# Optimization experiments

Measured on AMD Instinct MI355X. Metric: run time of the kernel, lower is better.

## Reference

```python
import jax, jax.numpy as jnp
import numpy as np

B, T, H = 16, 2048, 1024   # batch, time, hidden_dim
G, V, D = 2, 320, 128      # num_codebooks, codebook_size, codebook_dim
TAU = 1.0                  # gumbel-softmax temperature (forward default)
EPS = 1e-9


def setup_inputs() -> dict:
    key = jax.random.key(0)
    ks = jax.random.split(key, 6)
    return {
        "x": jax.random.normal(ks[0], (B, T, H), jnp.float32),
        "W_in": jax.random.normal(ks[1], (G * V, H), jnp.float32) / np.sqrt(H),
        "b_in": jnp.zeros((G * V,), jnp.float32),
        "codebook": jax.random.uniform(ks[2], (G, V, D), jnp.float32),
        "W_out": jax.random.normal(ks[3], (H, G * D), jnp.float32) / np.sqrt(G * D),
        "b_out": jnp.zeros((H,), jnp.float32),
        "gumbel_u": jax.random.uniform(ks[4], (B, T, G, V), jnp.float32,
                                       minval=1e-6, maxval=1.0 - 1e-6),
    }


def reference(x, W_in, b_in, codebook, W_out, b_out, gumbel_u):
    # input projection -> per-group logits [B,T,G,V]
    logits = (x @ W_in.T + b_in).reshape(B, T, G, V)
    # gumbel-softmax (soft, training path)
    gumbels = -jnp.log(-jnp.log(gumbel_u))
    probs = jax.nn.softmax((logits + gumbels) / TAU, axis=-1)
    # perplexity over average code usage
    avg_probs = probs.mean(axis=(0, 1))  # [G,V]
    perplexity = jnp.exp(-(avg_probs * jnp.log(avg_probs + EPS)).sum(-1)).mean()
    # quantize: soft mixture over codebook, concat groups, project out
    q = jnp.einsum('btgv,gvd->btgd', probs, codebook).reshape(B, T, G * D)
    q = q @ W_out.T + b_out  # [B,T,H]
    commit_loss = jnp.mean((x - jax.lax.stop_gradient(q)) ** 2)
    return (q, perplexity, commit_loss)
```

## Files before the change

### kernel.cpp

```cpp
#include <hip/hip_runtime.h>

typedef unsigned short ushort_t;
typedef unsigned int uint_t;
typedef __attribute__((ext_vector_type(4))) float f32x4;
typedef __attribute__((ext_vector_type(8))) short bf16x8;

#define B_   16
#define T_   2048
#define H_   1024
#define G_   2
#define V_   320
#define D_   128
#define NT   32768
#define GV   640
#define GD   256

#define LGKM0() asm volatile("s_waitcnt lgkmcnt(0)" ::: "memory")
#define BAR()   __builtin_amdgcn_s_barrier()
#define GLDS16(g, l) __builtin_amdgcn_global_load_lds( \
    (const __attribute__((address_space(1))) void*)(g), \
    (__attribute__((address_space(3))) void*)(l), 16, 0, 0)

__device__ __forceinline__ ushort_t cvt_bf16(float f) {
  uint_t u = __float_as_uint(f);
  uint_t r = (u + 0x7FFFu + ((u >> 16) & 1u)) >> 16;
  return (ushort_t)r;
}

__device__ __forceinline__ bf16x8 pack8(f32x4 a, f32x4 b) {
  union { uint_t u[4]; bf16x8 v; } r;
  asm("v_cvt_pk_bf16_f32 %0, %1, %2" : "=v"(r.u[0]) : "v"(a[0]), "v"(a[1]));
  asm("v_cvt_pk_bf16_f32 %0, %1, %2" : "=v"(r.u[1]) : "v"(a[2]), "v"(a[3]));
  asm("v_cvt_pk_bf16_f32 %0, %1, %2" : "=v"(r.u[2]) : "v"(b[0]), "v"(b[1]));
  asm("v_cvt_pk_bf16_f32 %0, %1, %2" : "=v"(r.u[3]) : "v"(b[2]), "v"(b[3]));
  return r.v;
}

__global__ void pq_prep(const float* __restrict__ W_in, const float* __restrict__ W_out,
                        const float* __restrict__ cb, ushort_t* __restrict__ winb,
                        ushort_t* __restrict__ woutb, ushort_t* __restrict__ cbp,
                        float* __restrict__ avg_g, float* __restrict__ closs,
                        uint_t* __restrict__ counter) {
  int idx = blockIdx.x * 256 + threadIdx.x;
  const int N1 = GV * H_;
  const int N2 = H_ * GD;
  const int N3 = 81920;
  if (idx < N1) { winb[idx] = cvt_bf16(W_in[idx]); return; }
  idx -= N1;
  if (idx < N2) { woutb[idx] = cvt_bf16(W_out[idx]); return; }
  idx -= N2;
  if (idx < N3) {
    int g = idx / 40960;
    int r = idx % 40960;
    int kk = r / 4096;
    int r2 = r % 4096;
    int n  = r2 >> 9;
    int ln = (r2 >> 3) & 63;
    int i  = r2 & 7;
    int v = kk * 32 + (ln >> 4) * 8 + i;
    int d = n * 16 + (ln & 15);
    cbp[idx] = cvt_bf16(cb[((size_t)g * V_ + v) * D_ + d]);
    return;
  }
  idx -= N3;
  if (idx < GV) { avg_g[idx] = 0.f; return; }
  idx -= GV;
  if (idx == 0) { *closs = 0.f; *counter = 0u; }
}

__global__ __launch_bounds__(256, 2) void pq_kA(
    const float* __restrict__ x, const float* __restrict__ b_in,
    const float* __restrict__ gum, const ushort_t* __restrict__ winb,
    const ushort_t* __restrict__ cbp, ushort_t* __restrict__ qmid,
    float* __restrict__ avg_g) {
  __shared__ char smem[43520];
  char* sBbuf = smem;
  char* sP    = smem;
  float* sAvg = (float*)(smem + 40960);

  const int tid = threadIdx.x;
  const int lane = tid & 63;
  const int wid = tid >> 6;
  const int wm = wid;
  const int g  = blockIdx.x & 1;
  const int lo = lane & 15;
  const int hi = lane >> 4;
  const int row0 = (blockIdx.x >> 1) * 128;

  for (int i = tid; i < V_; i += 256) sAvg[i] = 0.f;

  const int bV   = wid * 80 + (lane >> 2);
  const int bCc  = (lane & 3) ^ ((lane >> 3) & 3);
  const ushort_t* bSrc0 = winb + (size_t)(g * 320 + bV) * H_ + bCc * 8;

  const float* xr0 = x + (size_t)(row0 + wm * 32 + lo) * H_ + hi * 8;
  const float* xr1 = xr0 + (size_t)16 * H_;

  f32x4 acc[2][20];
#pragma unroll
  for (int m = 0; m < 2; ++m)
#pragma unroll
    for (int n = 0; n < 20; ++n) acc[m][n] = (f32x4){0.f, 0.f, 0.f, 0.f};

  __syncthreads();

#define STAGEB(buf, kb)                                                         \
  do {                                                                          \
    char* lb = sBbuf + (buf) * 20480 + wid * 5120;                              \
    const ushort_t* bs = bSrc0 + (kb);                                          \
    GLDS16(bs,             lb);                                                 \
    GLDS16(bs + 16 * H_,   lb + 1024);                                          \
    GLDS16(bs + 32 * H_,   lb + 2048);                                          \
    GLDS16(bs + 48 * H_,   lb + 3072);                                          \
    GLDS16(bs + 64 * H_,   lb + 4096);                                          \
  } while (0)

  STAGEB(0, 0);
  f32x4 xa0 = *reinterpret_cast<const f32x4*>(xr0);
  f32x4 xa1 = *reinterpret_cast<const f32x4*>(xr0 + 4);
  f32x4 xb0 = *reinterpret_cast<const f32x4*>(xr1);
  f32x4 xb1 = *reinterpret_cast<const f32x4*>(xr1 + 4);

  const int swzB = (lo >> 1) & 3;

#pragma unroll 1
  for (int ks = 0; ks < 32; ++ks) {
    if (ks < 31) {
      STAGEB((ks + 1) & 1, (ks + 1) * 32);
      asm volatile("s_waitcnt vmcnt(5)" ::: "memory");
    } else {
      asm volatile("s_waitcnt vmcnt(0)" ::: "memory");
    }
    BAR();

    bf16x8 af0 = pack8(xa0, xa1);
    bf16x8 af1 = pack8(xb0, xb1);

    if (ks < 31) {
      const int ko = (ks + 1) * 32;
      xa0 = *reinterpret_cast<const f32x4*>(xr0 + ko);
      xa1 = *reinterpret_cast<const f32x4*>(xr0 + ko + 4);
      xb0 = *reinterpret_cast<const f32x4*>(xr1 + ko);
      xb1 = *reinterpret_cast<const f32x4*>(xr1 + ko + 4);
    }

    const char* cB = sBbuf + (ks & 1) * 20480;
#pragma unroll
    for (int n = 0; n < 20; ++n) {
      const int v = n * 16 + lo;
      bf16x8 bf = *reinterpret_cast<const bf16x8*>(cB + v * 64 + ((hi ^ swzB) * 16));
      acc[0][n] = __builtin_amdgcn_mfma_f32_16x16x32_bf16(af0, bf, acc[0][n], 0, 0, 0);
      acc[1][n] = __builtin_amdgcn_mfma_f32_16x16x32_bf16(af1, bf, acc[1][n], 0, 0, 0);
    }
    LGKM0();
    BAR();
  }
#undef STAGEB

  float bias[20];
#pragma unroll
  for (int n = 0; n < 20; ++n) bias[n] = b_in[g * 320 + n * 16 + lo];

#pragma unroll
  for (int mrep = 0; mrep < 2; ++mrep) {
#pragma unroll
    for (int j = 0; j < 4; ++j) {
      const int trow = row0 + wm * 32 + mrep * 16 + hi * 4 + j;
      const float* up = gum + ((size_t)trow * G_ + g) * V_;
      float zmax = -3.0e38f;
#pragma unroll
      for (int n = 0; n < 20; ++n) {
        float u = up[n * 16 + lo];
        float gv = -__logf(-__logf(u));
        float z = acc[mrep][n][j] + bias[n] + gv;
        acc[mrep][n][j] = z;
        zmax = fmaxf(zmax, z);
      }
#pragma unroll
      for (int mk = 1; mk <= 8; mk <<= 1) zmax = fmaxf(zmax, __shfl_xor(zmax, mk));
      float s = 0.f;
#pragma unroll
      for (int n = 0; n < 20; ++n) {
        float p = __expf(acc[mrep][n][j] - zmax);
        acc[mrep][n][j] = p;
        s += p;
      }
#pragma unroll
      for (int mk = 1; mk <= 8; mk <<= 1) s += __shfl_xor(s, mk);
      float inv = 1.f / s;
#pragma unroll
      for (int n = 0; n < 20; ++n) acc[mrep][n][j] *= inv;
    }
#pragma unroll
    for (int n = 0; n < 20; ++n) {
      float cs = acc[mrep][n][0] + acc[mrep][n][1] + acc[mrep][n][2] + acc[mrep][n][3];
      cs += __shfl_xor(cs, 16);
      cs += __shfl_xor(cs, 32);
      if (hi == 0) atomicAdd(&sAvg[n * 16 + lo], cs);
    }
#pragma unroll
    for (int n = 0; n < 20; ++n) {
#pragma unroll
      for (int j = 0; j < 4; ++j) {
        float v = acc[mrep][n][j];
        float pv = __shfl_xor(v, 1);
        if ((lane & 1) == 0) {
          uint_t w = (uint_t)cvt_bf16(v) | ((uint_t)cvt_bf16(pv) << 16);
          int prow = wm * 16 + hi * 4 + j;
          int byte = prow * 640 + (((n * 16 + lo) * 2) ^ ((prow & 7) << 4));
          *reinterpret_cast<uint_t*>(sP + byte) = w;
        }
      }
    }
    LGKM0();
    f32x4 acc2[8];
#pragma unroll
    for (int n = 0; n < 8; ++n) acc2[n] = (f32x4){0.f, 0.f, 0.f, 0.f};
#pragma unroll
    for (int kk = 0; kk < 10; ++kk) {
      int prow = wm * 16 + lo;
      int byte = prow * 640 + ((kk * 64 + hi * 16) ^ ((prow & 7) << 4));
      bf16x8 ap = *reinterpret_cast<const bf16x8*>(sP + byte);
#pragma unroll
      for (int n = 0; n < 8; ++n) {
        bf16x8 bc = *reinterpret_cast<const bf16x8*>(cbp + ((size_t)((g * 10 + kk) * 8 + n) * 64 + lane) * 8);
        acc2[n] = __builtin_amdgcn_mfma_f32_16x16x32_bf16(ap, bc, acc2[n], 0, 0, 0);
      }
    }
#pragma unroll
    for (int n = 0; n < 8; ++n) {
#pragma unroll
      for (int j = 0; j < 4; ++j) {
        float v = acc2[n][j];
        float pv = __shfl_xor(v, 1);
        if ((lane & 1) == 0) {
          uint_t w = (uint_t)cvt_bf16(v) | ((uint_t)cvt_bf16(pv) << 16);
          int trow = row0 + wm * 32 + mrep * 16 + hi * 4 + j;
          *reinterpret_cast<uint_t*>(qmid + (size_t)trow * GD + g * 128 + n * 16 + lo) = w;
        }
      }
    }
  }
  __syncthreads();
  for (int i = tid; i < V_; i += 256) atomicAdd(&avg_g[g * 320 + i], sAvg[i]);
}

__global__ __launch_bounds__(512, 2) void pq_kB(
    const ushort_t* __restrict__ qmid, const ushort_t* __restrict__ woutb,
    const float* __restrict__ b_out, const float* __restrict__ x,
    float* __restrict__ out, float* __restrict__ closs,
    const float* __restrict__ avg_g, uint_t* __restrict__ counter) {
  __shared__ char smem[49152 + 64];
  __shared__ int sLast;
  char* sA = smem;
  char* sB = smem + 16384;
  float* sRed = (float*)(smem + 49152);

  const int tid = threadIdx.x;
  const int lane = tid & 63;
  const int wid = tid >> 6;
  const int wm = wid >> 2;
  const int wn = wid & 3;
  const int lo = lane & 15, hi = lane >> 4;
  const int tm = blockIdx.x >> 2;
  const int tn = blockIdx.x & 3;
  const int row0 = tm * 128;
  const int col0 = tn * 256;

  f32x4 acc[4][4];
#pragma unroll
  for (int mr = 0; mr < 4; ++mr)
#pragma unroll
    for (int nr = 0; nr < 4; ++nr) acc[mr][nr] = (f32x4){0.f, 0.f, 0.f, 0.f};

  for (int ks = 0; ks < 4; ++ks) {
    const int kb = ks * 64;
#pragma unroll
    for (int u = 0; u < 2; ++u) {
      int s = u * 512 + tid;
      int r = s >> 3, c = s & 7;
      uint4 wv = *reinterpret_cast<const uint4*>(qmid + (size_t)(row0 + r) * GD + kb + c * 8);
      int byte = (r * 128 + c * 16) ^ ((r & 7) << 4);
      *reinterpret_cast<uint4*>(sA + byte) = wv;
    }
#pragma unroll
    for (int u = 0; u < 4; ++u) {
      int s = u * 512 + tid;
      int r = s >> 3, c = s & 7;
      uint4 wv = *reinterpret_cast<const uint4*>(woutb + (size_t)(col0 + r) * GD + kb + c * 8);
      int byte = (r * 128 + c * 16) ^ ((r & 7) << 4);
      *reinterpret_cast<uint4*>(sB + byte) = wv;
    }
    __syncthreads();
#pragma unroll
    for (int kk = 0; kk < 2; ++kk) {
      bf16x8 af[4], bf[4];
#pragma unroll
      for (int mr = 0; mr < 4; ++mr) {
        int row = wm * 64 + mr * 16 + lo;
        int byte = (row * 128 + kk * 64 + hi * 16) ^ ((row & 7) << 4);
        af[mr] = *reinterpret_cast<const bf16x8*>(sA + byte);
      }
#pragma unroll
      for (int nr = 0; nr < 4; ++nr) {
        int col = wn * 64 + nr * 16 + lo;
        int byte = (col * 128 + kk * 64 + hi * 16) ^ ((col & 7) << 4);
        bf[nr] = *reinterpret_cast<const bf16x8*>(sB + byte);
      }
#pragma unroll
      for (int mr = 0; mr < 4; ++mr)
#pragma unroll
        for (int nr = 0; nr < 4; ++nr)
          acc[mr][nr] = __builtin_amdgcn_mfma_f32_16x16x32_bf16(af[mr], bf[nr], acc[mr][nr], 0, 0, 0);
    }
    __syncthreads();
  }
  float bias[4];
#pragma unroll
  for (int nr = 0; nr < 4; ++nr) bias[nr] = b_out[col0 + wn * 64 + nr * 16 + lo];
  float csum = 0.f;
#pragma unroll
  for (int mr = 0; mr < 4; ++mr)
#pragma unroll
    for (int nr = 0; nr < 4; ++nr)
#pragma unroll
      for (int j = 0; j < 4; ++j) {
        int row = row0 + wm * 64 + mr * 16 + hi * 4 + j;
        int col = col0 + wn * 64 + nr * 16 + lo;
        float q = acc[mr][nr][j] + bias[nr];
        out[(size_t)row * H_ + col] = q;
        float d = x[(size_t)row * H_ + col] - q;
        csum += d * d;
      }
#pragma unroll
  for (int mk = 1; mk <= 32; mk <<= 1) csum += __shfl_xor(csum, mk);
  if (lane == 0) sRed[wid] = csum;
  __syncthreads();
  if (tid == 0) {
    float t = 0.f;
    for (int w = 0; w < 8; ++w) t += sRed[w];
    atomicAdd(closs, t);
    __threadfence();
    uint_t c = atomicAdd(counter, 1u);
    sLast = (c == 1023u) ? 1 : 0;
  }
  __syncthreads();
  if (sLast && tid < 64) {
    float a0 = 0.f, a1 = 0.f;
    for (int v = tid; v < V_; v += 64) {
      float p0 = avg_g[v] * (1.f / (float)NT);
      a0 += p0 * __logf(p0 + 1e-9f);
      float p1 = avg_g[V_ + v] * (1.f / (float)NT);
      a1 += p1 * __logf(p1 + 1e-9f);
    }
#pragma unroll
    for (int mk = 1; mk <= 32; mk <<= 1) { a0 += __shfl_xor(a0, mk); a1 += __shfl_xor(a1, mk); }
    if (tid == 0) {
      float cl = atomicAdd(closs, 0.0f);
      out[(size_t)NT * H_]     = 0.5f * (__expf(-a0) + __expf(-a1));
      out[(size_t)NT * H_ + 1] = cl * (1.f / ((float)NT * (float)H_));
    }
  }
}

extern "C" void kernel_launch(void* const* d_in, const int* in_sizes, int n_in,
                              void* d_out, int out_size, void* d_ws, size_t ws_size,
                              hipStream_t stream) {
  const float* x     = (const float*)d_in[0];
  const float* W_in  = (const float*)d_in[1];
  const float* b_in  = (const float*)d_in[2];
  const float* cb    = (const float*)d_in[3];
  const float* W_out = (const float*)d_in[4];
  const float* b_out = (const float*)d_in[5];
  const float* gum   = (const float*)d_in[6];
  float* out = (float*)d_out;

  char* ws = (char*)d_ws;
  ushort_t* winb  = (ushort_t*)ws;
  ushort_t* woutb = (ushort_t*)(ws + 1310720);
  ushort_t* cbp   = (ushort_t*)(ws + 1835008);
  float*    avg_g = (float*)(ws + 1998848);
  float*    closs = (float*)(ws + 2001408);
  uint_t*   cnt   = (uint_t*)(ws + 2001472);
  ushort_t* qmid  = (ushort_t*)(ws + 2001920);

  pq_prep<<<3907, 256, 0, stream>>>(W_in, W_out, cb, winb, woutb, cbp, avg_g, closs, cnt);
  pq_kA<<<512, 256, 0, stream>>>(x, b_in, gum, winb, cbp, qmid, avg_g);
  pq_kB<<<1024, 512, 0, stream>>>(qmid, woutb, b_out, x, out, closs, avg_g, cnt);
}
```

Before: 245.1 us.

## Transpose logits MFMA so each lane owns one row for softmax

Swaps the MFMA operand order in the logits GEMM, so each lane now holds four consecutive vocab entries of a single token row instead of four rows. Softmax max and sum then need only two cross-lane shuffles per row, and the gumbel noise and bias are read as float4 vectors instead of scalar loads. Probabilities are packed straight to bf16 with v_cvt_pk into the swizzled LDS tile, with no shuffle-and-pair step. The column sums for avg_probs now take a 4-step shuffle reduction per element, which may add shuffle work in exchange.

```diff
diff --git a/kernel.cpp b/kernel.cpp
--- a/kernel.cpp
+++ b/kernel.cpp
@@ -27,12 +27,18 @@
   return (ushort_t)r;
 }
 
+__device__ __forceinline__ uint_t cvtpk(float a, float b) {
+  uint_t r;
+  asm("v_cvt_pk_bf16_f32 %0, %1, %2" : "=v"(r) : "v"(a), "v"(b));
+  return r;
+}
+
 __device__ __forceinline__ bf16x8 pack8(f32x4 a, f32x4 b) {
   union { uint_t u[4]; bf16x8 v; } r;
-  asm("v_cvt_pk_bf16_f32 %0, %1, %2" : "=v"(r.u[0]) : "v"(a[0]), "v"(a[1]));
-  asm("v_cvt_pk_bf16_f32 %0, %1, %2" : "=v"(r.u[1]) : "v"(a[2]), "v"(a[3]));
-  asm("v_cvt_pk_bf16_f32 %0, %1, %2" : "=v"(r.u[2]) : "v"(b[0]), "v"(b[1]));
-  asm("v_cvt_pk_bf16_f32 %0, %1, %2" : "=v"(r.u[3]) : "v"(b[2]), "v"(b[3]));
+  r.u[0] = cvtpk(a[0], a[1]);
+  r.u[1] = cvtpk(a[2], a[3]);
+  r.u[2] = cvtpk(b[0], b[1]);
+  r.u[3] = cvtpk(b[2], b[3]);
   return r.v;
 }
 
@@ -73,7 +79,7 @@
     const float* __restrict__ gum, const ushort_t* __restrict__ winb,
     const ushort_t* __restrict__ cbp, ushort_t* __restrict__ qmid,
     float* __restrict__ avg_g) {
-  __shared__ char smem[43520];
+  __shared__ char smem[42240];
   char* sBbuf = smem;
   char* sP    = smem;
   float* sAvg = (float*)(smem + 40960);
@@ -149,78 +155,91 @@
     for (int n = 0; n < 20; ++n) {
       const int v = n * 16 + lo;
       bf16x8 bf = *reinterpret_cast<const bf16x8*>(cB + v * 64 + ((hi ^ swzB) * 16));
-      acc[0][n] = __builtin_amdgcn_mfma_f32_16x16x32_bf16(af0, bf, acc[0][n], 0, 0, 0);
-      acc[1][n] = __builtin_amdgcn_mfma_f32_16x16x32_bf16(af1, bf, acc[1][n], 0, 0, 0);
+      acc[0][n] = __builtin_amdgcn_mfma_f32_16x16x32_bf16(bf, af0, acc[0][n], 0, 0, 0);
+      acc[1][n] = __builtin_amdgcn_mfma_f32_16x16x32_bf16(bf, af1, acc[1][n], 0, 0, 0);
     }
     LGKM0();
     BAR();
   }
 #undef STAGEB
 
-  float bias[20];
-#pragma unroll
-  for (int n = 0; n < 20; ++n) bias[n] = b_in[g * 320 + n * 16 + lo];
+  const float* bp = b_in + g * 320;
 
 #pragma unroll
   for (int mrep = 0; mrep < 2; ++mrep) {
-#pragma unroll
-    for (int j = 0; j < 4; ++j) {
-      const int trow = row0 + wm * 32 + mrep * 16 + hi * 4 + j;
-      const float* up = gum + ((size_t)trow * G_ + g) * V_;
-      float zmax = -3.0e38f;
-#pragma unroll
-      for (int n = 0; n < 20; ++n) {
-        float u = up[n * 16 + lo];
-        float gv = -__logf(-__logf(u));
-        float z = acc[mrep][n][j] + bias[n] + gv;
-        acc[mrep][n][j] = z;
-        zmax = fmaxf(zmax, z);
-      }
-#pragma unroll
-      for (int mk = 1; mk <= 8; mk <<= 1) zmax = fmaxf(zmax, __shfl_xor(zmax, mk));
-      float s = 0.f;
-#pragma unroll
-      for (int n = 0; n < 20; ++n) {
+    const int trow = row0 + wm * 32 + mrep * 16 + lo;
+    const float* up = gum + ((size_t)trow * G_ + g) * V_;
+
+    float zmax = -3.0e38f;
+#pragma unroll 4
+    for (int n = 0; n < 20; ++n) {
+      const float4 u4 = *reinterpret_cast<const float4*>(up + n * 16 + hi * 4);
+      const float4 b4 = *reinterpret_cast<const float4*>(bp + n * 16 + hi * 4);
+      float z0 = acc[mrep][n][0] + b4.x - __logf(-__logf(u4.x));
+      float z1 = acc[mrep][n][1] + b4.y - __logf(-__logf(u4.y));
+      float z2 = acc[mrep][n][2] + b4.z - __logf(-__logf(u4.z));
+      float z3 = acc[mrep][n][3] + b4.w - __logf(-__logf(u4.w));
+      acc[mrep][n][0] = z0; acc[mrep][n][1] = z1;
+      acc[mrep][n][2] = z2; acc[mrep][n][3] = z3;
+      zmax = fmaxf(zmax, fmaxf(fmaxf(z0, z1), fmaxf(z2, z3)));
+    }
+    zmax = fmaxf(zmax, __shfl_xor(zmax, 16));
+    zmax = fmaxf(zmax, __shfl_xor(zmax, 32));
+
+    float s = 0.f;
+#pragma unroll
+    for (int n = 0; n < 20; ++n) {
+#pragma unroll
+      for (int j = 0; j < 4; ++j) {
         float p = __expf(acc[mrep][n][j] - zmax);
         acc[mrep][n][j] = p;
         s += p;
       }
-#pragma unroll
-      for (int mk = 1; mk <= 8; mk <<= 1) s += __shfl_xor(s, mk);
-      float inv = 1.f / s;
-#pragma unroll
-      for (int n = 0; n < 20; ++n) acc[mrep][n][j] *= inv;
-    }
-#pragma unroll
-    for (int n = 0; n < 20; ++n) {
-      float cs = acc[mrep][n][0] + acc[mrep][n][1] + acc[mrep][n][2] + acc[mrep][n][3];
-      cs += __shfl_xor(cs, 16);
-      cs += __shfl_xor(cs, 32);
-      if (hi == 0) atomicAdd(&sAvg[n * 16 + lo], cs);
-    }
+    }
+    s += __shfl_xor(s, 16);
+    s += __shfl_xor(s, 32);
+    const float inv = 1.f / s;
+#pragma unroll
+    for (int n = 0; n < 20; ++n)
+#pragma unroll
+      for (int j = 0; j < 4; ++j) acc[mrep][n][j] *= inv;
+
 #pragma unroll
     for (int n = 0; n < 20; ++n) {
 #pragma unroll
       for (int j = 0; j < 4; ++j) {
         float v = acc[mrep][n][j];
-        float pv = __shfl_xor(v, 1);
-        if ((lane & 1) == 0) {
-          uint_t w = (uint_t)cvt_bf16(v) | ((uint_t)cvt_bf16(pv) << 16);
-          int prow = wm * 16 + hi * 4 + j;
-          int byte = prow * 640 + (((n * 16 + lo) * 2) ^ ((prow & 7) << 4));
-          *reinterpret_cast<uint_t*>(sP + byte) = w;
-        }
+        v += __shfl_xor(v, 1);
+        v += __shfl_xor(v, 2);
+        v += __shfl_xor(v, 4);
+        v += __shfl_xor(v, 8);
+        if ((lane & 15) == 0) atomicAdd(&sAvg[n * 16 + hi * 4 + j], v);
+      }
+    }
+
+    {
+      const int row = wm * 16 + lo;
+      char* rp = sP + row * 640 + 8 * (hi & 1);
+      const int rx = row & 7;
+#pragma unroll
+      for (int n = 0; n < 20; ++n) {
+        uint_t w0 = cvtpk(acc[mrep][n][0], acc[mrep][n][1]);
+        uint_t w1 = cvtpk(acc[mrep][n][2], acc[mrep][n][3]);
+        const int chunk = (2 * n + (hi >> 1)) ^ rx;
+        *reinterpret_cast<uint_t*>(rp + chunk * 16)     = w0;
+        *reinterpret_cast<uint_t*>(rp + chunk * 16 + 4) = w1;
       }
     }
     LGKM0();
+
     f32x4 acc2[8];
 #pragma unroll
     for (int n = 0; n < 8; ++n) acc2[n] = (f32x4){0.f, 0.f, 0.f, 0.f};
 #pragma unroll
     for (int kk = 0; kk < 10; ++kk) {
-      int prow = wm * 16 + lo;
-      int byte = prow * 640 + ((kk * 64 + hi * 16) ^ ((prow & 7) << 4));
-      bf16x8 ap = *reinterpret_cast<const bf16x8*>(sP + byte);
+      const int row = wm * 16 + lo;
+      const int chunk = (4 * kk + hi) ^ (row & 7);
+      bf16x8 ap = *reinterpret_cast<const bf16x8*>(sP + row * 640 + chunk * 16);
 #pragma unroll
       for (int n = 0; n < 8; ++n) {
         bf16x8 bc = *reinterpret_cast<const bf16x8*>(cbp + ((size_t)((g * 10 + kk) * 8 + n) * 64 + lane) * 8);
@@ -235,8 +254,8 @@
         float pv = __shfl_xor(v, 1);
         if ((lane & 1) == 0) {
           uint_t w = (uint_t)cvt_bf16(v) | ((uint_t)cvt_bf16(pv) << 16);
-          int trow = row0 + wm * 32 + mrep * 16 + hi * 4 + j;
-          *reinterpret_cast<uint_t*>(qmid + (size_t)trow * GD + g * 128 + n * 16 + lo) = w;
+          int tr = row0 + wm * 32 + mrep * 16 + hi * 4 + j;
+          *reinterpret_cast<uint_t*>(qmid + (size_t)tr * GD + g * 128 + n * 16 + lo) = w;
         }
       }
     }
```

New measurement: 371.1 us. 51.4% more time.
